# Optimization experiments

Measured on AMD Instinct MI355X. Metric: run time of the kernel, lower is better.

The kernel has to match this reference:

```python
import jax, jax.numpy as jnp
import numpy as np

BN_EPS = 1e-5

def batchnorm(x, gamma, beta):
    # training-mode BN over axis 0 with biased variance (matches torch)
    mean = jnp.mean(x, axis=0)
    var = jnp.var(x, axis=0)
    return (x - mean) * jax.lax.rsqrt(var + BN_EPS) * gamma + beta

def setup_inputs() -> dict:
    key = jax.random.key(0)
    ks = jax.random.split(key, 8)
    N, M, A, B = 50000, 12, 64, 41
    atom_in_fea = jax.random.normal(ks[0], (N, A), dtype=jnp.float32)
    nbr_fea = jax.random.normal(ks[1], (N, M, B), dtype=jnp.float32)
    nbr_fea_idx = jax.random.randint(ks[2], (N, M), 0, N)
    fan_in = 2 * A + B
    lim = 1.0 / np.sqrt(fan_in)
    W = jax.random.uniform(ks[3], (2 * A, fan_in), minval=-lim, maxval=lim, dtype=jnp.float32)
    b = jax.random.uniform(ks[4], (2 * A,), minval=-lim, maxval=lim, dtype=jnp.float32)
    bn1_g = jnp.ones((2 * A,), jnp.float32)
    bn1_b = jnp.zeros((2 * A,), jnp.float32)
    bn2_g = jnp.ones((A,), jnp.float32)
    bn2_b = jnp.zeros((A,), jnp.float32)
    return {"atom_in_fea": atom_in_fea, "nbr_fea": nbr_fea, "nbr_fea_idx": nbr_fea_idx,
            "W": W, "b": b, "bn1_g": bn1_g, "bn1_b": bn1_b, "bn2_g": bn2_g, "bn2_b": bn2_b}

def reference(atom_in_fea, nbr_fea, nbr_fea_idx, W, b, bn1_g, bn1_b, bn2_g, bn2_b):
    N, M = nbr_fea_idx.shape
    A = atom_in_fea.shape[1]
    atom_nbr_fea = atom_in_fea[nbr_fea_idx]                       # (N, M, A) gather
    self_fea = jnp.broadcast_to(atom_in_fea[:, None, :], (N, M, A))
    total_nbr_fea = jnp.concatenate([self_fea, atom_nbr_fea, nbr_fea], axis=2)  # (N,M,2A+B)
    total_gated = jnp.einsum('nmf,of->nmo', total_nbr_fea, W) + b  # (N,M,2A)
    total_gated = batchnorm(total_gated.reshape(-1, 2 * A), bn1_g, bn1_b).reshape(N, M, 2 * A)
    nbr_filter, nbr_core = total_gated[..., :A], total_gated[..., A:]
    nbr_sumed = jnp.sum(jax.nn.sigmoid(nbr_filter) * jax.nn.softplus(nbr_core), axis=1)  # (N,A)
    nbr_sumed = batchnorm(nbr_sumed, bn2_g, bn2_b)
    return jax.nn.softplus(atom_in_fea + nbr_sumed)
```

## Files before the change

### kernel.cpp

```cpp
#include <hip/hip_runtime.h>
#include <math.h>

#define N_ATOMS 50000
#define M_NBR   12
#define A_FEA   64
#define B_FEA   41
#define KF      169
#define KP      192
#define LDA     200
#define OC      128
#define NROW    600000
#define TR32    32
#define NT32    18750
#define NT192   3125
#define S2S     68
#define BN_EPS  1e-5f
#define L2E     1.44269504088896340736f
#define LN2     0.693147180559945309417f

#define WS_SUM1   0
#define WS_SUMSQ1 128
#define WS_SUM2   256
#define WS_SUMSQ2 320
#define WS_NFLOAT 384
#define WS_GATED_OFF 2048ull
#define GATED_BYTES  ((size_t)NT32 * 512 * 16)

typedef __attribute__((ext_vector_type(8))) short s16x8;
typedef __attribute__((ext_vector_type(4))) float f32x4;

__device__ __forceinline__ float fsigmoid(float x) {
    float e = __builtin_amdgcn_exp2f(-x * L2E);
    return __builtin_amdgcn_rcpf(1.f + e);
}
__device__ __forceinline__ float fsoftplus(float x) {
    float e = __builtin_amdgcn_exp2f(-fabsf(x) * L2E);
    return fmaxf(x, 0.f) + __builtin_amdgcn_logf(1.f + e) * LN2;
}
__device__ __forceinline__ unsigned short f2bf(float f) {
    unsigned int u = __float_as_uint(f);
    u += 0x7FFFu + ((u >> 16) & 1u);
    return (unsigned short)(u >> 16);
}
__device__ __forceinline__ unsigned int pack2bf(float lo, float hi) {
    return (unsigned int)f2bf(lo) | ((unsigned int)f2bf(hi) << 16);
}
__device__ __forceinline__ float bf_lo(unsigned int u) { return __uint_as_float(u << 16); }
__device__ __forceinline__ float bf_hi(unsigned int u) { return __uint_as_float(u & 0xFFFF0000u); }

__global__ void k_zero_stats(float* __restrict__ stats) {
    int i = blockIdx.x * blockDim.x + threadIdx.x;
    if (i < WS_NFLOAT) stats[i] = 0.f;
}
__global__ void k_zero(float* __restrict__ dout, float* __restrict__ stats) {
    int i = blockIdx.x * blockDim.x + threadIdx.x;
    int stride = gridDim.x * blockDim.x;
    for (int j = i; j < N_ATOMS * A_FEA; j += stride) dout[j] = 0.f;
    if (i < WS_NFLOAT) stats[i] = 0.f;
}

struct TileRegs {
    float4 selfv[2];
    float4 gat[2];
    float4 bond0, bond1;
};

__device__ __forceinline__ void issue_selfbond(TileRegs& R, const float* __restrict__ atom,
                                               const float* __restrict__ nbr,
                                               int rb, int r16, int k4, int tid) {
#pragma unroll
    for (int it = 0; it < 2; ++it) {
        int row = rb + r16 + it * 16;
        R.selfv[it] = *(const float4*)(atom + ((unsigned)row / 12u) * A_FEA + k4);
    }
    const float* bb = nbr + (size_t)rb * B_FEA;
    R.bond0 = *(const float4*)(bb + (size_t)tid * 4);
    if (tid < 72) R.bond1 = *(const float4*)(bb + (size_t)(256 + tid) * 4);
}
__device__ __forceinline__ void issue_gat(TileRegs& R, const float* __restrict__ atom,
                                          const int nbi[2], int k4) {
#pragma unroll
    for (int it = 0; it < 2; ++it)
        R.gat[it] = *(const float4*)(atom + (unsigned)nbi[it] * A_FEA + k4);
}
__device__ __forceinline__ void write_tile(unsigned short* __restrict__ At,
                                           const TileRegs& R, int r16, int k4, int tid) {
#pragma unroll
    for (int it = 0; it < 2; ++it) {
        int r = r16 + it * 16;
        uint2 u;
        u.x = pack2bf(R.selfv[it].x, R.selfv[it].y);
        u.y = pack2bf(R.selfv[it].z, R.selfv[it].w);
        *(uint2*)&At[r * LDA + k4] = u;
        uint2 v;
        v.x = pack2bf(R.gat[it].x, R.gat[it].y);
        v.y = pack2bf(R.gat[it].z, R.gat[it].w);
        *(uint2*)&At[r * LDA + A_FEA + k4] = v;
    }
    {
        const float bv[4] = {R.bond0.x, R.bond0.y, R.bond0.z, R.bond0.w};
#pragma unroll
        for (int e = 0; e < 4; ++e) {
            int le = tid * 4 + e;
            unsigned r = (unsigned)le / 41u, j = (unsigned)le - r * 41u;
            At[r * LDA + 2 * A_FEA + j] = f2bf(bv[e]);
        }
    }
    if (tid < 72) {
        const float bv[4] = {R.bond1.x, R.bond1.y, R.bond1.z, R.bond1.w};
#pragma unroll
        for (int e = 0; e < 4; ++e) {
            int le = 1024 + tid * 4 + e;
            unsigned r = (unsigned)le / 41u, j = (unsigned)le - r * 41u;
            At[r * LDA + 2 * A_FEA + j] = f2bf(bv[e]);
        }
    }
}

template <bool STORE>
__global__ __launch_bounds__(256, 3)
void k_gemm_spill(const float* __restrict__ atom, const float* __restrict__ nbr,
                  const int* __restrict__ idx, const float* __restrict__ W,
                  float* __restrict__ stats, uint4* __restrict__ gated) {
    __shared__ __align__(16) unsigned short At[2][TR32 * LDA];
    const int tid = threadIdx.x;
    for (int i = tid; i < 2 * TR32 * (KP - KF); i += 256) {
        int b  = i / (TR32 * (KP - KF));
        int ii = i - b * (TR32 * (KP - KF));
        int r  = ii / (KP - KF);
        int j  = KF + ii - r * (KP - KF);
        At[b][r * LDA + j] = 0;
    }
    const int lane = tid & 63, gg = tid >> 6;
    const int col  = lane & 15, q8 = (lane >> 4) * 8;
    const int r16  = tid >> 4;
    const int k4   = (tid & 15) * 4;

    s16x8 bfr[2][6];
#pragma unroll
    for (int tt = 0; tt < 2; ++tt) {
        const float* wr = W + ((gg + tt * 4) * 16 + col) * KF;
#pragma unroll
        for (int kc = 0; kc < 6; ++kc) {
            int kb = kc * 32 + q8;
            s16x8 f;
#pragma unroll
            for (int j = 0; j < 8; ++j) {
                int k = kb + j;
                f[j] = (short)f2bf(k < KF ? wr[k] : 0.f);
            }
            bfr[tt][kc] = f;
        }
    }

    const int per = (NT32 + gridDim.x - 1) / gridDim.x;
    const int tA = blockIdx.x * per;
    const int tB = min(NT32, tA + per);

    float s[2] = {0.f, 0.f}, q[2] = {0.f, 0.f};
    TileRegs R;
    int nbiN[2];
    if (tA < tB) {
        int rb = tA * TR32;
        int nbiC[2] = {idx[rb + r16], idx[rb + r16 + 16]};
        issue_selfbond(R, atom, nbr, rb, r16, k4, tid);
        issue_gat(R, atom, nbiC, k4);
        if (tA + 1 < tB) {
            int rb1 = rb + TR32;
            nbiN[0] = idx[rb1 + r16]; nbiN[1] = idx[rb1 + r16 + 16];
        }
    }
    int p = 0;
    for (int t = tA; t < tB; ++t) {
        write_tile(At[p], R, r16, k4, tid);
        if (t + 1 < tB) {
            issue_selfbond(R, atom, nbr, (t + 1) * TR32, r16, k4, tid);
            issue_gat(R, atom, nbiN, k4);
            if (t + 2 < tB) {
                int rb2 = (t + 2) * TR32;
                nbiN[0] = idx[rb2 + r16]; nbiN[1] = idx[rb2 + r16 + 16];
            }
        }
        __syncthreads();
        const unsigned short* A = At[p];
        f32x4 acc[2][2];
#pragma unroll
        for (int rt = 0; rt < 2; ++rt)
#pragma unroll
            for (int tt = 0; tt < 2; ++tt) acc[rt][tt] = (f32x4){0.f, 0.f, 0.f, 0.f};
#pragma unroll
        for (int kc = 0; kc < 6; ++kc) {
            const int k0 = kc * 32;
            const s16x8 a0 = *(const s16x8*)&A[(col) * LDA + k0 + q8];
            const s16x8 a1 = *(const s16x8*)&A[(16 + col) * LDA + k0 + q8];
#pragma unroll
            for (int tt = 0; tt < 2; ++tt) {
                acc[0][tt] = __builtin_amdgcn_mfma_f32_16x16x32_bf16(a0, bfr[tt][kc], acc[0][tt], 0, 0, 0);
                acc[1][tt] = __builtin_amdgcn_mfma_f32_16x16x32_bf16(a1, bfr[tt][kc], acc[1][tt], 0, 0, 0);
            }
        }
#pragma unroll
        for (int tt = 0; tt < 2; ++tt)
#pragma unroll
            for (int rt = 0; rt < 2; ++rt)
#pragma unroll
                for (int e = 0; e < 4; ++e) {
                    float v = acc[rt][tt][e];
                    s[tt] += v; q[tt] = fmaf(v, v, q[tt]);
                }
        if (STORE) {
#pragma unroll
            for (int rt = 0; rt < 2; ++rt) {
                uint4 u;
                u.x = pack2bf(acc[rt][0][0], acc[rt][0][1]);
                u.y = pack2bf(acc[rt][0][2], acc[rt][0][3]);
                u.z = pack2bf(acc[rt][1][0], acc[rt][1][1]);
                u.w = pack2bf(acc[rt][1][2], acc[rt][1][3]);
                gated[(size_t)t * 512 + rt * 256 + tid] = u;
            }
        }
        p ^= 1;
    }
#pragma unroll
    for (int tt = 0; tt < 2; ++tt) {
        float sv = s[tt], qv = q[tt];
        sv += __shfl_xor(sv, 16); sv += __shfl_xor(sv, 32);
        qv += __shfl_xor(qv, 16); qv += __shfl_xor(qv, 32);
        if (lane < 16) {
            int c = (gg + tt * 4) * 16 + col;
            atomicAdd(&stats[WS_SUM1 + c], sv);
            atomicAdd(&stats[WS_SUMSQ1 + c], qv);
        }
    }
}

__global__ __launch_bounds__(256, 3)
void k_apply(const uint4* __restrict__ gated,
             const float* __restrict__ g1, const float* __restrict__ b1,
             float* __restrict__ stats, float* __restrict__ dout) {
    __shared__ float S2[192 * S2S];
    const int tid = threadIdx.x, lane = tid & 63;
    const int col = lane & 15, quad = lane >> 4, gg = tid >> 6;
    const int cF = gg * 16 + col, cC = cF + 64;

    const float invn = 1.f / (float)NROW;
    float meanF = stats[WS_SUM1 + cF] * invn;
    float varF  = stats[WS_SUMSQ1 + cF] * invn - meanF * meanF;
    float scF   = g1[cF] * rsqrtf(varF + BN_EPS), shF = b1[cF] - meanF * scF;
    float meanC = stats[WS_SUM1 + cC] * invn;
    float varC  = stats[WS_SUMSQ1 + cC] * invn - meanC * meanC;
    float scC   = g1[cC] * rsqrtf(varC + BN_EPS), shC = b1[cC] - meanC * scC;

    float bs = 0.f, bq = 0.f;
    for (int T = blockIdx.x; T < NT192; T += gridDim.x) {
        __syncthreads();
        uint4 G[6][2];
#pragma unroll
        for (int sub = 0; sub < 6; ++sub) {
            const size_t base = (size_t)(T * 6 + sub) * 512 + tid;
#pragma unroll
            for (int rt = 0; rt < 2; ++rt)
                G[sub][rt] = gated[base + rt * 256];
        }
#pragma unroll
        for (int sub = 0; sub < 6; ++sub)
#pragma unroll
            for (int rt = 0; rt < 2; ++rt) {
                const uint4 u = G[sub][rt];
                const float fv[4] = {bf_lo(u.x), bf_hi(u.x), bf_lo(u.y), bf_hi(u.y)};
                const float cv[4] = {bf_lo(u.z), bf_hi(u.z), bf_lo(u.w), bf_hi(u.w)};
#pragma unroll
                for (int e = 0; e < 4; ++e) {
                    float gF = fmaf(fv[e], scF, shF);
                    float gC = fmaf(cv[e], scC, shC);
                    float v  = fsigmoid(gF) * fsoftplus(gC);
                    int row = sub * 32 + rt * 16 + quad * 4 + e;
                    S2[row * S2S + cF] = v;
                }
            }
        __syncthreads();
#pragma unroll
        for (int j = 0; j < 4; ++j) {
            int lin = tid + j * 256;
            int a = lin >> 6, c = lin & 63;
            const float* pp = &S2[(a * 12) * S2S + c];
            float sum = 0.f;
#pragma unroll
            for (int m = 0; m < 12; ++m) sum += pp[m * S2S];
            dout[((size_t)T * 16 + a) * 64 + c] = sum;
            bs += sum; bq = fmaf(sum, sum, bq);
        }
    }
    __syncthreads();
    S2[tid] = bs; S2[256 + tid] = bq;
    __syncthreads();
    if (tid < 64) {
        float ss = S2[tid] + S2[tid + 64] + S2[tid + 128] + S2[tid + 192];
        float qq = S2[256 + tid] + S2[256 + tid + 64] + S2[256 + tid + 128] + S2[256 + tid + 192];
        atomicAdd(&stats[WS_SUM2 + tid], ss);
        atomicAdd(&stats[WS_SUMSQ2 + tid], qq);
    }
}

__global__ __launch_bounds__(256, 2)
void k_gemm_main(const float* __restrict__ atom, const float* __restrict__ nbr,
                 const int* __restrict__ idx, const float* __restrict__ W,
                 const float* __restrict__ g1, const float* __restrict__ b1,
                 const float* __restrict__ stats, float* __restrict__ dout) {
    __shared__ __align__(16) unsigned short At[TR32 * LDA];
    __shared__ float S[4 * 64];
    const int tid = threadIdx.x;
    for (int i = tid; i < TR32 * (KP - KF); i += 256) {
        int r = i / (KP - KF), j = KF + i - r * (KP - KF);
        At[r * LDA + j] = 0;
    }
    for (int i = tid; i < 4 * 64; i += 256) S[i] = 0.f;
    const int lane = tid & 63, gg = tid >> 6;
    const int col = lane & 15, q8 = (lane >> 4) * 8, quad = lane >> 4;
    const int r16 = tid >> 4, k4 = (tid & 15) * 4;

    s16x8 bfr[2][6];
#pragma unroll
    for (int tt = 0; tt < 2; ++tt) {
        const float* wr = W + ((gg + tt * 4) * 16 + col) * KF;
#pragma unroll
        for (int kc = 0; kc < 6; ++kc) {
            int kb = kc * 32 + q8;
            s16x8 f;
#pragma unroll
            for (int j = 0; j < 8; ++j) { int k = kb + j; f[j] = (short)f2bf(k < KF ? wr[k] : 0.f); }
            bfr[tt][kc] = f;
        }
    }
    const float invn = 1.f / (float)NROW;
    float sc[2], sh[2];
#pragma unroll
    for (int tt = 0; tt < 2; ++tt) {
        int c = (gg + tt * 4) * 16 + col;
        float mean = stats[WS_SUM1 + c] * invn;
        float var  = stats[WS_SUMSQ1 + c] * invn - mean * mean;
        sc[tt] = g1[c] * rsqrtf(var + BN_EPS);
        sh[tt] = b1[c] - mean * sc[tt];
    }
    const int per = (NT32 + gridDim.x - 1) / gridDim.x;
    const int tA = blockIdx.x * per, tB = min(NT32, tA + per);
    for (int t = tA; t < tB; ++t) {
        const int rb = t * TR32;
        __syncthreads();
        {
            TileRegs R;
            int nbiC[2] = {idx[rb + r16], idx[rb + r16 + 16]};
            issue_selfbond(R, atom, nbr, rb, r16, k4, tid);
            issue_gat(R, atom, nbiC, k4);
            write_tile(At, R, r16, k4, tid);
        }
        __syncthreads();
        f32x4 acc[2][2];
#pragma unroll
        for (int rt = 0; rt < 2; ++rt)
#pragma unroll
            for (int tt = 0; tt < 2; ++tt) acc[rt][tt] = (f32x4){0.f, 0.f, 0.f, 0.f};
#pragma unroll
        for (int kc = 0; kc < 6; ++kc) {
            const int k0 = kc * 32;
            const s16x8 a0 = *(const s16x8*)&At[(col) * LDA + k0 + q8];
            const s16x8 a1 = *(const s16x8*)&At[(16 + col) * LDA + k0 + q8];
#pragma unroll
            for (int tt = 0; tt < 2; ++tt) {
                acc[0][tt] = __builtin_amdgcn_mfma_f32_16x16x32_bf16(a0, bfr[tt][kc], acc[0][tt], 0, 0, 0);
                acc[1][tt] = __builtin_amdgcn_mfma_f32_16x16x32_bf16(a1, bfr[tt][kc], acc[1][tt], 0, 0, 0);
            }
        }
        const int a0i = rb / M_NBR;
#pragma unroll
        for (int rt = 0; rt < 2; ++rt)
#pragma unroll
            for (int e = 0; e < 4; ++e) {
                float gF = fmaf(acc[rt][0][e], sc[0], sh[0]);
                float gC = fmaf(acc[rt][1][e], sc[1], sh[1]);
                float v  = fsigmoid(gF) * fsoftplus(gC);
                int row = rb + rt * 16 + quad * 4 + e;
                atomicAdd(&S[(row / M_NBR - a0i) * 64 + gg * 16 + col], v);
            }
        __syncthreads();
        const int amax = (rb + TR32 - 1) / M_NBR - a0i;
        for (int i = tid; i < 4 * 64; i += 256) {
            float v = S[i];
            S[i] = 0.f;
            int a = i >> 6;
            if (a <= amax) atomicAdd(&dout[(a0i + a) * 64 + (i & 63)], v);
        }
    }
}

__global__ __launch_bounds__(256, 1)
void k_bn2_stats(const float* __restrict__ dout, float* __restrict__ stats) {
    int tid = threadIdx.x;
    int c = tid & 63;
    int g = tid >> 6;
    float s = 0.f, q = 0.f;
    for (int n = blockIdx.x * 4 + g; n < N_ATOMS; n += gridDim.x * 4) {
        float v = dout[n * 64 + c];
        s += v; q = fmaf(v, v, q);
    }
    __shared__ float red[4][64];
    red[g][c] = s;
    __syncthreads();
    if (g == 0)
        atomicAdd(&stats[WS_SUM2 + c], red[0][c] + red[1][c] + red[2][c] + red[3][c]);
    __syncthreads();
    red[g][c] = q;
    __syncthreads();
    if (g == 0)
        atomicAdd(&stats[WS_SUMSQ2 + c], red[0][c] + red[1][c] + red[2][c] + red[3][c]);
}

__global__ void k_final(const float* __restrict__ atom, const float* __restrict__ g2,
                        const float* __restrict__ b2, const float* __restrict__ stats,
                        float* __restrict__ dout) {
    int i0 = blockIdx.x * blockDim.x + threadIdx.x;
    int c = i0 & 63;
    const float invn = 1.f / (float)N_ATOMS;
    float mean = stats[WS_SUM2 + c] * invn;
    float var  = stats[WS_SUMSQ2 + c] * invn - mean * mean;
    float sc   = g2[c] * rsqrtf(var + BN_EPS);
    float sh   = b2[c] - mean * sc;
    int stride = gridDim.x * blockDim.x;
    for (int i = i0; i < N_ATOMS * A_FEA; i += stride) {
        float v = fmaf(dout[i], sc, sh) + atom[i];
        dout[i] = fsoftplus(v);
    }
}

extern "C" void kernel_launch(void* const* d_in, const int* in_sizes, int n_in,
                              void* d_out, int out_size, void* d_ws, size_t ws_size,
                              hipStream_t stream) {
    const float* atom = (const float*)d_in[0];
    const float* nbr  = (const float*)d_in[1];
    const int*   idx  = (const int*)d_in[2];
    const float* W    = (const float*)d_in[3];
    const float* g1   = (const float*)d_in[5];
    const float* b1   = (const float*)d_in[6];
    const float* g2   = (const float*)d_in[7];
    const float* b2   = (const float*)d_in[8];
    float* dout  = (float*)d_out;
    float* stats = (float*)d_ws;
    uint4* gated = (uint4*)((char*)d_ws + WS_GATED_OFF);

    const bool fused = ws_size >= (WS_GATED_OFF + GATED_BYTES);

    if (fused) {
        k_zero_stats<<<2, 256, 0, stream>>>(stats);
        k_gemm_spill<true><<<750, 256, 0, stream>>>(atom, nbr, idx, W, stats, gated);
        k_apply<<<625, 256, 0, stream>>>(gated, g1, b1, stats, dout);
        k_final<<<512, 256, 0, stream>>>(atom, g2, b2, stats, dout);
    } else {
        k_zero<<<512, 256, 0, stream>>>(dout, stats);
        k_gemm_spill<false><<<750, 256, 0, stream>>>(atom, nbr, idx, W, stats, nullptr);
        k_gemm_main<<<1024, 256, 0, stream>>>(atom, nbr, idx, W, g1, b1, stats, dout);
        k_bn2_stats<<<256, 256, 0, stream>>>(dout, stats);
        k_final<<<512, 256, 0, stream>>>(atom, g2, b2, stats, dout);
    }
}
```

Baseline: 259.3 us.

## Deepen prefetch pipelines in gated GEMM and BN apply kernels

The gated GEMM kernel now keeps two tiles of gathered self/neighbor/bond data in flight, using two register sets, and prefetches neighbor indices four tiles ahead instead of two. The apply kernel double-buffers its gated-tile loads, fetching the next tile's bf16 data into registers while the current one is processed. Both changes aim to hide global and gather memory latency behind compute. The cost is much higher register pressure, which at the given launch bounds may cause spills or lower occupancy.

```diff
diff --git a/kernel.cpp b/kernel.cpp
--- a/kernel.cpp
+++ b/kernel.cpp
@@ -158,69 +158,88 @@
     const int tB = min(NT32, tA + per);
 
     float s[2] = {0.f, 0.f}, q[2] = {0.f, 0.f};
-    TileRegs R;
-    int nbiN[2];
+    TileRegs RA, RB;
+    int nbiQ0[2], nbiQ1[2];
     if (tA < tB) {
         int rb = tA * TR32;
-        int nbiC[2] = {idx[rb + r16], idx[rb + r16 + 16]};
-        issue_selfbond(R, atom, nbr, rb, r16, k4, tid);
-        issue_gat(R, atom, nbiC, k4);
-        if (tA + 1 < tB) {
-            int rb1 = rb + TR32;
-            nbiN[0] = idx[rb1 + r16]; nbiN[1] = idx[rb1 + r16 + 16];
-        }
-    }
+        int nb[2] = {idx[rb + r16], idx[rb + r16 + 16]};
+        issue_selfbond(RA, atom, nbr, rb, r16, k4, tid);
+        issue_gat(RA, atom, nb, k4);
+    }
+    if (tA + 1 < tB) {
+        int rb = (tA + 1) * TR32;
+        int nb[2] = {idx[rb + r16], idx[rb + r16 + 16]};
+        issue_selfbond(RB, atom, nbr, rb, r16, k4, tid);
+        issue_gat(RB, atom, nb, k4);
+    }
+    if (tA + 2 < tB) { int rb = (tA + 2) * TR32; nbiQ0[0] = idx[rb + r16]; nbiQ0[1] = idx[rb + r16 + 16]; }
+    if (tA + 3 < tB) { int rb = (tA + 3) * TR32; nbiQ1[0] = idx[rb + r16]; nbiQ1[1] = idx[rb + r16 + 16]; }
+
     int p = 0;
-    for (int t = tA; t < tB; ++t) {
-        write_tile(At[p], R, r16, k4, tid);
-        if (t + 1 < tB) {
-            issue_selfbond(R, atom, nbr, (t + 1) * TR32, r16, k4, tid);
-            issue_gat(R, atom, nbiN, k4);
-            if (t + 2 < tB) {
-                int rb2 = (t + 2) * TR32;
-                nbiN[0] = idx[rb2 + r16]; nbiN[1] = idx[rb2 + r16 + 16];
-            }
-        }
-        __syncthreads();
-        const unsigned short* A = At[p];
-        f32x4 acc[2][2];
-#pragma unroll
-        for (int rt = 0; rt < 2; ++rt)
-#pragma unroll
-            for (int tt = 0; tt < 2; ++tt) acc[rt][tt] = (f32x4){0.f, 0.f, 0.f, 0.f};
-#pragma unroll
-        for (int kc = 0; kc < 6; ++kc) {
-            const int k0 = kc * 32;
-            const s16x8 a0 = *(const s16x8*)&A[(col) * LDA + k0 + q8];
-            const s16x8 a1 = *(const s16x8*)&A[(16 + col) * LDA + k0 + q8];
-#pragma unroll
-            for (int tt = 0; tt < 2; ++tt) {
-                acc[0][tt] = __builtin_amdgcn_mfma_f32_16x16x32_bf16(a0, bfr[tt][kc], acc[0][tt], 0, 0, 0);
-                acc[1][tt] = __builtin_amdgcn_mfma_f32_16x16x32_bf16(a1, bfr[tt][kc], acc[1][tt], 0, 0, 0);
-            }
-        }
-#pragma unroll
-        for (int tt = 0; tt < 2; ++tt)
-#pragma unroll
-            for (int rt = 0; rt < 2; ++rt)
-#pragma unroll
-                for (int e = 0; e < 4; ++e) {
-                    float v = acc[rt][tt][e];
-                    s[tt] += v; q[tt] = fmaf(v, v, q[tt]);
-                }
-        if (STORE) {
-#pragma unroll
-            for (int rt = 0; rt < 2; ++rt) {
-                uint4 u;
-                u.x = pack2bf(acc[rt][0][0], acc[rt][0][1]);
-                u.y = pack2bf(acc[rt][0][2], acc[rt][0][3]);
-                u.z = pack2bf(acc[rt][1][0], acc[rt][1][1]);
-                u.w = pack2bf(acc[rt][1][2], acc[rt][1][3]);
-                gated[(size_t)t * 512 + rt * 256 + tid] = u;
-            }
-        }
-        p ^= 1;
-    }
+
+#define GEMM_STEP(Rc, NQ, t)                                                     \
+    do {                                                                         \
+        write_tile(At[p], Rc, r16, k4, tid);       \
+        if ((t) + 2 < tB) {                          \
+            issue_selfbond(Rc, atom, nbr, ((t) + 2) * TR32, r16, k4, tid);       \
+            issue_gat(Rc, atom, NQ, k4);                                         \
+        }                                                                        \
+        if ((t) + 4 < tB) {                       \
+            int rb4 = ((t) + 4) * TR32;                                          \
+            NQ[0] = idx[rb4 + r16]; NQ[1] = idx[rb4 + r16 + 16];                 \
+        }                                                                        \
+        __syncthreads();                                                         \
+        {                                                                        \
+            const unsigned short* A = At[p];                                     \
+            f32x4 acc[2][2];                                                     \
+            _Pragma("unroll")                                                    \
+            for (int rt = 0; rt < 2; ++rt)                                       \
+                _Pragma("unroll")                                                \
+                for (int tt = 0; tt < 2; ++tt) acc[rt][tt] = (f32x4){0.f, 0.f, 0.f, 0.f}; \
+            _Pragma("unroll")                                                    \
+            for (int kc = 0; kc < 6; ++kc) {                                     \
+                const int k0 = kc * 32;                                          \
+                const s16x8 a0 = *(const s16x8*)&A[(col) * LDA + k0 + q8];       \
+                const s16x8 a1 = *(const s16x8*)&A[(16 + col) * LDA + k0 + q8];  \
+                _Pragma("unroll")                                                \
+                for (int tt = 0; tt < 2; ++tt) {                                 \
+                    acc[0][tt] = __builtin_amdgcn_mfma_f32_16x16x32_bf16(a0, bfr[tt][kc], acc[0][tt], 0, 0, 0); \
+                    acc[1][tt] = __builtin_amdgcn_mfma_f32_16x16x32_bf16(a1, bfr[tt][kc], acc[1][tt], 0, 0, 0); \
+                }                                                                \
+            }                                                                    \
+            _Pragma("unroll")                                                    \
+            for (int tt = 0; tt < 2; ++tt)                                       \
+                _Pragma("unroll")                                                \
+                for (int rt = 0; rt < 2; ++rt)                                   \
+                    _Pragma("unroll")                                            \
+                    for (int e = 0; e < 4; ++e) {                                \
+                        float v = acc[rt][tt][e];                                \
+                        s[tt] += v; q[tt] = fmaf(v, v, q[tt]);                   \
+                    }                                                            \
+            if (STORE) {                                                         \
+                _Pragma("unroll")                                                \
+                for (int rt = 0; rt < 2; ++rt) {                                 \
+                    uint4 u;                                                     \
+                    u.x = pack2bf(acc[rt][0][0], acc[rt][0][1]);                 \
+                    u.y = pack2bf(acc[rt][0][2], acc[rt][0][3]);                 \
+                    u.z = pack2bf(acc[rt][1][0], acc[rt][1][1]);                 \
+                    u.w = pack2bf(acc[rt][1][2], acc[rt][1][3]);                 \
+                    gated[(size_t)(t) * 512 + rt * 256 + tid] = u;               \
+                }                                                                \
+            }                                                                    \
+        }                                                                        \
+        p ^= 1;                                                                  \
+          \
+          \
+                              \
+    } while (0)
+
+    for (int t = tA; t < tB; t += 2) {
+        GEMM_STEP(RA, nbiQ0, t);
+        if (t + 1 < tB) GEMM_STEP(RB, nbiQ1, t + 1);
+    }
+#undef GEMM_STEP
+
 #pragma unroll
     for (int tt = 0; tt < 2; ++tt) {
         float sv = s[tt], qv = q[tt];
@@ -251,22 +270,33 @@
     float varC  = stats[WS_SUMSQ1 + cC] * invn - meanC * meanC;
     float scC   = g1[cC] * rsqrtf(varC + BN_EPS), shC = b1[cC] - meanC * scC;
 
+    uint4 Gc[6][2], Gn[6][2];
+    if (blockIdx.x < NT192) {
+#pragma unroll
+        for (int sub = 0; sub < 6; ++sub) {
+            const size_t base = (size_t)(blockIdx.x * 6 + sub) * 512 + tid;
+#pragma unroll
+            for (int rt = 0; rt < 2; ++rt) Gc[sub][rt] = gated[base + rt * 256];
+        }
+    }
+
     float bs = 0.f, bq = 0.f;
     for (int T = blockIdx.x; T < NT192; T += gridDim.x) {
+        const int Tn = T + gridDim.x;
+        if (Tn < NT192) {
+#pragma unroll
+            for (int sub = 0; sub < 6; ++sub) {
+                const size_t base = (size_t)(Tn * 6 + sub) * 512 + tid;
+#pragma unroll
+                for (int rt = 0; rt < 2; ++rt) Gn[sub][rt] = gated[base + rt * 256];
+            }
+        }
         __syncthreads();
-        uint4 G[6][2];
-#pragma unroll
-        for (int sub = 0; sub < 6; ++sub) {
-            const size_t base = (size_t)(T * 6 + sub) * 512 + tid;
-#pragma unroll
-            for (int rt = 0; rt < 2; ++rt)
-                G[sub][rt] = gated[base + rt * 256];
-        }
 #pragma unroll
         for (int sub = 0; sub < 6; ++sub)
 #pragma unroll
             for (int rt = 0; rt < 2; ++rt) {
-                const uint4 u = G[sub][rt];
+                const uint4 u = Gc[sub][rt];
                 const float fv[4] = {bf_lo(u.x), bf_hi(u.x), bf_lo(u.y), bf_hi(u.y)};
                 const float cv[4] = {bf_lo(u.z), bf_hi(u.z), bf_lo(u.w), bf_hi(u.w)};
 #pragma unroll
@@ -289,6 +319,12 @@
             for (int m = 0; m < 12; ++m) sum += pp[m * S2S];
             dout[((size_t)T * 16 + a) * 64 + c] = sum;
             bs += sum; bq = fmaf(sum, sum, bq);
+        }
+        if (Tn < NT192) {
+#pragma unroll
+            for (int sub = 0; sub < 6; ++sub)
+#pragma unroll
+                for (int rt = 0; rt < 2; ++rt) Gc[sub][rt] = Gn[sub][rt];
         }
     }
     __syncthreads();
```

After: 268.0 us. +3.4%, slower.

## Sum neighbor gates in registers in apply kernel, drop LDS transpose

Applied to the files above, without the earlier changes.

The apply kernel now has each thread load exactly the gated tiles belonging to one (atom, channel) pair, so the 12-neighbor sum is accumulated in registers. This removes the 192x68 shared-memory staging buffer and the two barriers per tile. The GEMM kernel also spreads tiles evenly across blocks instead of using ceil-division, and replaces __syncthreads with a raw lgkmcnt wait plus s_barrier. The new gather pattern reads 16-byte elements with a channel-dependent stride, which may coalesce less well than the old contiguous loads.

```diff
diff --git a/kernel.cpp b/kernel.cpp
--- a/kernel.cpp
+++ b/kernel.cpp
@@ -13,7 +13,6 @@
 #define TR32    32
 #define NT32    18750
 #define NT192   3125
-#define S2S     68
 #define BN_EPS  1e-5f
 #define L2E     1.44269504088896340736f
 #define LN2     0.693147180559945309417f
@@ -25,6 +24,8 @@
 #define WS_NFLOAT 384
 #define WS_GATED_OFF 2048ull
 #define GATED_BYTES  ((size_t)NT32 * 512 * 16)
+
+#define BAR_LGKM() asm volatile("s_waitcnt lgkmcnt(0)\n\ts_barrier" ::: "memory")
 
 typedef __attribute__((ext_vector_type(8))) short s16x8;
 typedef __attribute__((ext_vector_type(4))) float f32x4;
@@ -153,9 +154,11 @@
         }
     }
 
-    const int per = (NT32 + gridDim.x - 1) / gridDim.x;
-    const int tA = blockIdx.x * per;
-    const int tB = min(NT32, tA + per);
+    const int base = NT32 / gridDim.x;
+    const int rem  = NT32 % gridDim.x;
+    const int bid  = blockIdx.x;
+    const int tA   = bid * base + min(bid, rem);
+    const int tB   = tA + base + (bid < rem ? 1 : 0);
 
     float s[2] = {0.f, 0.f}, q[2] = {0.f, 0.f};
     TileRegs R;
@@ -181,7 +184,7 @@
                 nbiN[0] = idx[rb2 + r16]; nbiN[1] = idx[rb2 + r16 + 16];
             }
         }
-        __syncthreads();
+        BAR_LGKM();
         const unsigned short* A = At[p];
         f32x4 acc[2][2];
 #pragma unroll
@@ -238,65 +241,60 @@
 void k_apply(const uint4* __restrict__ gated,
              const float* __restrict__ g1, const float* __restrict__ b1,
              float* __restrict__ stats, float* __restrict__ dout) {
-    __shared__ float S2[192 * S2S];
-    const int tid = threadIdx.x, lane = tid & 63;
-    const int col = lane & 15, quad = lane >> 4, gg = tid >> 6;
-    const int cF = gg * 16 + col, cC = cF + 64;
+    __shared__ float red[512];
+    const int tid = threadIdx.x;
+    const int c   = tid & 63;
+    const int w   = tid >> 6;
+    const int col = c & 15, gg = c >> 4;
 
     const float invn = 1.f / (float)NROW;
-    float meanF = stats[WS_SUM1 + cF] * invn;
-    float varF  = stats[WS_SUMSQ1 + cF] * invn - meanF * meanF;
-    float scF   = g1[cF] * rsqrtf(varF + BN_EPS), shF = b1[cF] - meanF * scF;
-    float meanC = stats[WS_SUM1 + cC] * invn;
-    float varC  = stats[WS_SUMSQ1 + cC] * invn - meanC * meanC;
-    float scC   = g1[cC] * rsqrtf(varC + BN_EPS), shC = b1[cC] - meanC * scC;
+    float meanF = stats[WS_SUM1 + c] * invn;
+    float varF  = stats[WS_SUMSQ1 + c] * invn - meanF * meanF;
+    float scF   = g1[c] * rsqrtf(varF + BN_EPS), shF = b1[c] - meanF * scF;
+    const int cc = c + 64;
+    float meanC = stats[WS_SUM1 + cc] * invn;
+    float varC  = stats[WS_SUMSQ1 + cc] * invn - meanC * meanC;
+    float scC   = g1[cc] * rsqrtf(varC + BN_EPS), shC = b1[cc] - meanC * scC;
 
     float bs = 0.f, bq = 0.f;
     for (int T = blockIdx.x; T < NT192; T += gridDim.x) {
-        __syncthreads();
-        uint4 G[6][2];
-#pragma unroll
-        for (int sub = 0; sub < 6; ++sub) {
-            const size_t base = (size_t)(T * 6 + sub) * 512 + tid;
-#pragma unroll
-            for (int rt = 0; rt < 2; ++rt)
-                G[sub][rt] = gated[base + rt * 256];
-        }
-#pragma unroll
-        for (int sub = 0; sub < 6; ++sub)
-#pragma unroll
-            for (int rt = 0; rt < 2; ++rt) {
-                const uint4 u = G[sub][rt];
+        uint4 G[4][3];
+#pragma unroll
+        for (int j = 0; j < 4; ++j) {
+            const int a = j * 4 + w;
+#pragma unroll
+            for (int l = 0; l < 3; ++l) {
+                const int Gi  = 3 * a + l;
+                const int sub = Gi >> 3, rt = (Gi >> 2) & 1, q = Gi & 3;
+                G[j][l] = gated[(size_t)(T * 6 + sub) * 512 + rt * 256
+                                + gg * 64 + q * 16 + col];
+            }
+        }
+#pragma unroll
+        for (int j = 0; j < 4; ++j) {
+            float sum = 0.f;
+#pragma unroll
+            for (int l = 0; l < 3; ++l) {
+                const uint4 u = G[j][l];
                 const float fv[4] = {bf_lo(u.x), bf_hi(u.x), bf_lo(u.y), bf_hi(u.y)};
                 const float cv[4] = {bf_lo(u.z), bf_hi(u.z), bf_lo(u.w), bf_hi(u.w)};
 #pragma unroll
                 for (int e = 0; e < 4; ++e) {
                     float gF = fmaf(fv[e], scF, shF);
                     float gC = fmaf(cv[e], scC, shC);
-                    float v  = fsigmoid(gF) * fsoftplus(gC);
-                    int row = sub * 32 + rt * 16 + quad * 4 + e;
-                    S2[row * S2S + cF] = v;
+                    sum += fsigmoid(gF) * fsoftplus(gC);
                 }
             }
-        __syncthreads();
-#pragma unroll
-        for (int j = 0; j < 4; ++j) {
-            int lin = tid + j * 256;
-            int a = lin >> 6, c = lin & 63;
-            const float* pp = &S2[(a * 12) * S2S + c];
-            float sum = 0.f;
-#pragma unroll
-            for (int m = 0; m < 12; ++m) sum += pp[m * S2S];
+            const int a = j * 4 + w;
             dout[((size_t)T * 16 + a) * 64 + c] = sum;
             bs += sum; bq = fmaf(sum, sum, bq);
         }
     }
-    __syncthreads();
-    S2[tid] = bs; S2[256 + tid] = bq;
+    red[tid] = bs; red[256 + tid] = bq;
     __syncthreads();
     if (tid < 64) {
-        float ss = S2[tid] + S2[tid + 64] + S2[tid + 128] + S2[tid + 192];
-        float qq = S2[256 + tid] + S2[256 + tid + 64] + S2[256 + tid + 128] + S2[256 + tid + 192];
+        float ss = red[tid] + red[tid + 64] + red[tid + 128] + red[tid + 192];
+        float qq = red[256 + tid] + red[256 + tid + 64] + red[256 + tid + 128] + red[256 + tid + 192];
         atomicAdd(&stats[WS_SUM2 + tid], ss);
         atomicAdd(&stats[WS_SUMSQ2 + tid], qq);
     }
```

After: 255.8 us. Within noise of the previous version (-1.3%).
